# Performance work log

Measured on AMD Instinct MI355X. Metric: run time of the kernel, lower is better.

The kernel has to match this reference:

```python
import jax, jax.numpy as jnp
import numpy as np

B, T, U, L, C = 2048, 100, 512, 3, 10


def setup_inputs() -> dict:
    key = jax.random.key(0)
    ks = jax.random.split(key, 2 + 3 * L + 2)
    x = jax.random.normal(ks[0], (B, T, 1), dtype=jnp.float32)
    mask = jax.random.randint(ks[1], (B, T), 0, 2) > 0
    inp = {"x": x, "mask": mask}
    in_dim = 1
    s = 2
    for l in range(L):
        # Keras LSTM kernel layout: gates ordered [i, f, g(candidate), o]
        inp[f"W{l}"] = jax.random.normal(ks[s], (in_dim, 4 * U), dtype=jnp.float32) * 0.05
        inp[f"U{l}"] = jax.random.normal(ks[s + 1], (U, 4 * U), dtype=jnp.float32) * 0.05
        b = np.zeros((4 * U,), dtype=np.float32)
        b[U:2 * U] = 1.0  # unit_forget_bias (Keras default)
        inp[f"b{l}"] = jnp.asarray(b)
        in_dim = U
        s += 2
    inp["Wd"] = jax.random.normal(ks[s], (U, C), dtype=jnp.float32) * 0.05
    inp["bd"] = jnp.zeros((C,), dtype=jnp.float32)
    return inp


def _lstm_step(x_t, h, c, W, Uw, b):
    z = x_t @ W + h @ Uw + b  # [B, 4U]
    i, f, g, o = jnp.split(z, 4, axis=-1)
    i = jax.nn.sigmoid(i)
    f = jax.nn.sigmoid(f)
    g = jnp.tanh(g)
    o = jax.nn.sigmoid(o)
    c_new = f * c + i * g
    h_new = o * jnp.tanh(c_new)
    return h_new, c_new


def reference(x, mask, W0, U0, b0, W1, U1, b1, W2, U2, b2, Wd, bd):
    params = [(W0, U0, b0), (W1, U1, b1), (W2, U2, b2)]
    xt = jnp.swapaxes(x, 0, 1)        # [T, B, 1]
    mt = jnp.swapaxes(mask, 0, 1)     # [T, B]
    Bsz = x.shape[0]
    init = tuple((jnp.zeros((Bsz, U), x.dtype), jnp.zeros((Bsz, U), x.dtype)) for _ in range(L))

    def scan_fn(carry, inp_t):
        x_t, m_t = inp_t
        m = m_t[:, None]  # [B, 1]
        new_states = []
        layer_in = x_t
        for (h, c), (W, Uw, b) in zip(carry, params):
            h_new, c_new = _lstm_step(layer_in, h, c, W, Uw, b)
            # Keras mask semantics: masked steps carry state/output forward
            h_new = jnp.where(m, h_new, h)
            c_new = jnp.where(m, c_new, c)
            new_states.append((h_new, c_new))
            layer_in = h_new
        return tuple(new_states), None

    final, _ = jax.lax.scan(scan_fn, init, (xt, mt))
    h_top = final[-1][0]  # [B, U]
    logits = h_top @ Wd + bd
    return jax.nn.softmax(logits, axis=-1)
```

## Files before the change

kernel.cpp:

```cpp
#include <hip/hip_runtime.h>
#include <cstdint>
#include <cstddef>

#define B_   2048
#define T_   100
#define U_   512
#define NG_  2048
#define C_   10

typedef __attribute__((ext_vector_type(8))) short   short8;
typedef __attribute__((ext_vector_type(4))) float   floatx4;
typedef unsigned short ushort_t;

__device__ inline ushort_t f2bf(float f){
  unsigned u = __float_as_uint(f);
  unsigned r = (u + 0x7FFFu + ((u >> 16) & 1u)) >> 16;
  return (ushort_t)r;
}
__device__ inline float bf2f(ushort_t b){ return __uint_as_float(((unsigned)b) << 16); }

__device__ inline float sigm(float x){ return 1.0f / (1.0f + __expf(-x)); }
__device__ inline float tanh_fast(float x){
  float a = fabsf(x);
  float e = __expf(-2.0f * a);
  float r = (1.0f - e) / (1.0f + e);
  return copysignf(r, x);
}

__device__ inline int orig_col(int p){
  int Tt  = p >> 7;
  int loc = p & 127;
  int half = loc >> 6;
  int loc2 = loc & 63;
  int gate = loc2 >> 4;
  int uu   = (half << 4) | (loc2 & 15);
  return gate * U_ + Tt * 32 + uu;
}

#define AS1(p) ((const __attribute__((address_space(1))) void*)(p))
#define AS3(p) ((__attribute__((address_space(3))) void*)(p))

__global__ void convert_weights(
    const float* __restrict__ W0, const float* __restrict__ U0, const float* __restrict__ b0,
    const float* __restrict__ W1, const float* __restrict__ U1, const float* __restrict__ b1,
    const float* __restrict__ W2, const float* __restrict__ U2, const float* __restrict__ b2,
    ushort_t* __restrict__ Bt0, ushort_t* __restrict__ Bt1, ushort_t* __restrict__ Bt2,
    float* __restrict__ W0p, float* __restrict__ biasp)
{
  const int N0 = NG_ * 512;
  const int N1 = NG_ * 1024;
  const int total = N0 + 2 * N1 + NG_ + 3 * NG_;
  int idx = blockIdx.x * 256 + threadIdx.x;
  if (idx >= total) return;

  if (idx < N0){
    int p = idx >> 9, k = idx & 511;
    Bt0[idx] = f2bf(U0[(size_t)k * NG_ + orig_col(p)]);
  } else if (idx < N0 + N1){
    int j = idx - N0; int p = j >> 10, k = j & 1023;
    int oc = orig_col(p);
    float v = (k < 512) ? W1[(size_t)k * NG_ + oc] : U1[(size_t)(k - 512) * NG_ + oc];
    Bt1[j] = f2bf(v);
  } else if (idx < N0 + 2 * N1){
    int j = idx - N0 - N1; int p = j >> 10, k = j & 1023;
    int oc = orig_col(p);
    float v = (k < 512) ? W2[(size_t)k * NG_ + oc] : U2[(size_t)(k - 512) * NG_ + oc];
    Bt2[j] = f2bf(v);
  } else if (idx < N0 + 2 * N1 + NG_){
    int p = idx - N0 - 2 * N1;
    W0p[p] = W0[orig_col(p)];
  } else {
    int j = idx - N0 - 2 * N1 - NG_;
    int l = j >> 11, p = j & 2047;
    const float* bs = (l == 0) ? b0 : (l == 1) ? b1 : b2;
    biasp[j] = bs[orig_col(p)];
  }
}

template<int LAYER>
__device__ __forceinline__ void do_task(
    const ushort_t* __restrict__ A0,
    const ushort_t* __restrict__ A1,
    const ushort_t* __restrict__ Bt,
    const float* __restrict__ biasp,
    const float* __restrict__ W0p,
    const float* __restrict__ x,
    const int* __restrict__ mask,
    float* __restrict__ cbuf,
    const ushort_t* __restrict__ hprev,
    ushort_t* __restrict__ hout,
    int t, int mt, int nt,
    ushort_t* tA, ushort_t* tB)
{
  constexpr int NPHASE = (LAYER == 0) ? 1 : 2;
  constexpr bool IS_L0 = (LAYER == 0);
  constexpr int K = NPHASE * 512;

  const int tid  = threadIdx.x;
  const int wv   = tid >> 6;
  const int lane = tid & 63;
  const int qd   = lane >> 4;
  const int l16  = lane & 15;
  const int wave_m = wv >> 1;
  const int wave_n = wv & 1;
  const int m0 = mt * 128, n0 = nt * 128;

  int srow[4], scol[4];
  #pragma unroll
  for (int cc2 = 0; cc2 < 4; ++cc2){
    int i = cc2 * 256 + wv * 64 + lane;
    srow[cc2] = i >> 3;
    scol[cc2] = ((i & 7) + (i >> 3)) & 7;
  }

  int aoff[2][4], boff[2][4];
  #pragma unroll
  for (int ks = 0; ks < 2; ++ks){
    #pragma unroll
    for (int w = 0; w < 4; ++w){
      int Ra = wave_m * 64 + w * 16 + l16;
      int Rb = wave_n * 64 + w * 16 + l16;
      int q  = ks * 4 + qd;
      aoff[ks][w] = Ra * 64 + ((q - Ra) & 7) * 8;
      boff[ks][w] = Rb * 64 + ((q - Rb) & 7) * 8;
    }
  }

  floatx4 acc[4][4];
  #pragma unroll
  for (int i = 0; i < 4; ++i)
    #pragma unroll
    for (int j = 0; j < 4; ++j) acc[i][j] = (floatx4){0.f, 0.f, 0.f, 0.f};

  #pragma unroll
  for (int ph = 0; ph < NPHASE; ++ph){
    const ushort_t* A = (NPHASE == 2 && ph == 1) ? A1 : A0;
    for (int k0 = 0; k0 < 512; k0 += 64){
      #pragma unroll
      for (int cc2 = 0; cc2 < 4; ++cc2){
        int ibase = cc2 * 256 + wv * 64;
        const ushort_t* ga = A + (size_t)(m0 + srow[cc2]) * U_ + k0 + scol[cc2] * 8;
        __builtin_amdgcn_global_load_lds(AS1(ga), AS3(&tA[ibase * 8]), 16, 0, 0);
        const ushort_t* gb = Bt + (size_t)(n0 + srow[cc2]) * K + ph * 512 + k0 + scol[cc2] * 8;
        __builtin_amdgcn_global_load_lds(AS1(gb), AS3(&tB[ibase * 8]), 16, 0, 0);
      }
      __syncthreads();

      #pragma unroll
      for (int ks = 0; ks < 2; ++ks){
        short8 af[4], bfr[4];
        #pragma unroll
        for (int wm = 0; wm < 4; ++wm)
          af[wm] = *(const short8*)&tA[aoff[ks][wm]];
        #pragma unroll
        for (int wn = 0; wn < 4; ++wn)
          bfr[wn] = *(const short8*)&tB[boff[ks][wn]];
        #pragma unroll
        for (int wm = 0; wm < 4; ++wm)
          #pragma unroll
          for (int wn = 0; wn < 4; ++wn)
            acc[wm][wn] = __builtin_amdgcn_mfma_f32_16x16x32_bf16(af[wm], bfr[wn], acc[wm][wn], 0, 0, 0);
      }
      __syncthreads();
    }
  }

  const int u  = nt * 32 + wave_n * 16 + l16;
  const int pb = nt * 128 + wave_n * 64 + l16;
  const float bi = biasp[pb], bf_ = biasp[pb + 16], bg = biasp[pb + 32], bo = biasp[pb + 48];
  float wi = 0.f, wf = 0.f, wg = 0.f, wo = 0.f;
  if (IS_L0){ wi = W0p[pb]; wf = W0p[pb + 16]; wg = W0p[pb + 32]; wo = W0p[pb + 48]; }

  #pragma unroll
  for (int wm = 0; wm < 4; ++wm){
    #pragma unroll
    for (int reg = 0; reg < 4; ++reg){
      int b = m0 + wave_m * 64 + wm * 16 + qd * 4 + reg;
      float zi = acc[wm][0][reg] + bi;
      float zf = acc[wm][1][reg] + bf_;
      float zg = acc[wm][2][reg] + bg;
      float zo = acc[wm][3][reg] + bo;
      if (IS_L0){
        float xv = x[(size_t)b * T_ + t];
        zi += xv * wi; zf += xv * wf; zg += xv * wg; zo += xv * wo;
      }
      int mk = mask[(size_t)b * T_ + t];
      size_t su = (size_t)b * U_ + u;
      float c_old = cbuf[su];
      float i_ = sigm(zi), f_ = sigm(zf), g_ = tanh_fast(zg), o_ = sigm(zo);
      float c_new = f_ * c_old + i_ * g_;
      float h_new = o_ * tanh_fast(c_new);
      ushort_t hb = mk ? f2bf(h_new) : hprev[su];
      cbuf[su] = mk ? c_new : c_old;
      hout[su] = hb;
    }
  }
}

__global__ __launch_bounds__(256, 3) void lstm_phase(
    const ushort_t* __restrict__ Bt0, const ushort_t* __restrict__ Bt1,
    const ushort_t* __restrict__ Bt2, const float* __restrict__ biasp,
    const float* __restrict__ W0p, const float* __restrict__ x,
    const int* __restrict__ mask,
    ushort_t* h00, ushort_t* h01, ushort_t* h10, ushort_t* h11,
    ushort_t* h20, ushort_t* h21,
    float* c0, float* c1, float* c2,
    int s)
{
  __shared__ __align__(16) ushort_t tA[128 * 64];
  __shared__ __align__(16) ushort_t tB[128 * 64];

  const int lin  = blockIdx.x;
  const int task = lin >> 8;
  const int tile = lin & 255;
  const int mt = tile >> 4, nt = tile & 15;

  ushort_t* h0[2] = {h00, h01};
  ushort_t* h1[2] = {h10, h11};
  ushort_t* h2[2] = {h20, h21};

  if (task == 0){
    if (s >= 100) return;
    int t = s, p = t & 1;
    do_task<0>(h0[p], nullptr, Bt0, biasp, W0p, x, mask,
               c0, h0[p], h0[p ^ 1], t, mt, nt, tA, tB);
  } else if (task == 1){
    if (s < 1 || s > 100) return;
    int t = s - 1, p = t & 1;
    do_task<1>(h0[p ^ 1], h1[p], Bt1, biasp + NG_, nullptr, x, mask,
               c1, h1[p], h1[p ^ 1], t, mt, nt, tA, tB);
  } else {
    if (s < 2) return;
    int t = s - 2, p = t & 1;
    do_task<2>(h1[p ^ 1], h2[p], Bt2, biasp + 2 * NG_, nullptr, x, mask,
               c2, h2[p], h2[p ^ 1], t, mt, nt, tA, tB);
  }
}

__global__ __launch_bounds__(256) void head_softmax(
    const ushort_t* __restrict__ h2, const float* __restrict__ Wd,
    const float* __restrict__ bd, float* __restrict__ out)
{
  int wv = threadIdx.x >> 6, lane = threadIdx.x & 63;
  int row = blockIdx.x * 4 + wv;
  const ushort_t* hr = h2 + (size_t)row * U_;

  float acc[C_];
  #pragma unroll
  for (int c = 0; c < C_; ++c) acc[c] = 0.f;

  short8 hv = *(const short8*)&hr[lane * 8];
  #pragma unroll
  for (int j = 0; j < 8; ++j){
    float hf = bf2f((ushort_t)hv[j]);
    int k = lane * 8 + j;
    #pragma unroll
    for (int c = 0; c < C_; ++c) acc[c] += hf * Wd[k * C_ + c];
  }
  #pragma unroll
  for (int c = 0; c < C_; ++c){
    float v = acc[c];
    #pragma unroll
    for (int off = 32; off > 0; off >>= 1) v += __shfl_xor(v, off);
    acc[c] = v + bd[c];
  }
  float mx = acc[0];
  #pragma unroll
  for (int c = 1; c < C_; ++c) mx = fmaxf(mx, acc[c]);
  float e[C_]; float s = 0.f;
  #pragma unroll
  for (int c = 0; c < C_; ++c){ e[c] = __expf(acc[c] - mx); s += e[c]; }
  float inv = 1.0f / s;
  if (lane == 0){
    #pragma unroll
    for (int c = 0; c < C_; ++c) out[(size_t)row * C_ + c] = e[c] * inv;
  }
}

extern "C" void kernel_launch(void* const* d_in, const int* in_sizes, int n_in,
                              void* d_out, int out_size, void* d_ws, size_t ws_size,
                              hipStream_t stream)
{
  const float* x  = (const float*)d_in[0];
  const int*  mask= (const int*)  d_in[1];
  const float* W0 = (const float*)d_in[2];
  const float* U0 = (const float*)d_in[3];
  const float* b0 = (const float*)d_in[4];
  const float* W1 = (const float*)d_in[5];
  const float* U1 = (const float*)d_in[6];
  const float* b1 = (const float*)d_in[7];
  const float* W2 = (const float*)d_in[8];
  const float* U2 = (const float*)d_in[9];
  const float* b2 = (const float*)d_in[10];
  const float* Wd = (const float*)d_in[11];
  const float* bd = (const float*)d_in[12];
  float* out = (float*)d_out;

  char* ws = (char*)d_ws;
  size_t off = 0;
  auto alloc = [&](size_t sz) -> char* {
    char* p = ws + off; off = (off + sz + 255) & ~(size_t)255; return p;
  };
  ushort_t* Bt0  = (ushort_t*)alloc((size_t)NG_ * 512 * 2);
  ushort_t* Bt1  = (ushort_t*)alloc((size_t)NG_ * 1024 * 2);
  ushort_t* Bt2  = (ushort_t*)alloc((size_t)NG_ * 1024 * 2);
  float*    W0p  = (float*)alloc((size_t)NG_ * 4);
  float*    biasp= (float*)alloc((size_t)3 * NG_ * 4);

  const size_t hsz = (size_t)B_ * U_ * 2;
  const size_t csz = (size_t)B_ * U_ * 4;
  char* state = alloc(6 * hsz + 3 * csz);
  ushort_t* hb[3][2]; float* cb[3];
  {
    char* pp = state;
    for (int l = 0; l < 3; ++l)
      for (int par = 0; par < 2; ++par){ hb[l][par] = (ushort_t*)pp; pp += hsz; }
    for (int l = 0; l < 3; ++l){ cb[l] = (float*)pp; pp += csz; }
  }

  hipMemsetAsync(state, 0, 6 * hsz + 3 * csz, stream);

  const int total = NG_ * 512 + 2 * NG_ * 1024 + NG_ + 3 * NG_;
  convert_weights<<<(total + 255) / 256, 256, 0, stream>>>(
      W0, U0, b0, W1, U1, b1, W2, U2, b2, Bt0, Bt1, Bt2, W0p, biasp);

  for (int s = 0; s < 102; ++s){
    lstm_phase<<<768, 256, 0, stream>>>(
        Bt0, Bt1, Bt2, biasp, W0p, x, mask,
        hb[0][0], hb[0][1], hb[1][0], hb[1][1], hb[2][0], hb[2][1],
        cb[0], cb[1], cb[2], s);
  }

  head_softmax<<<B_ / 4, 256, 0, stream>>>(hb[2][0], Wd, bd, out);
}
```

Before: 3.480 ms.

## Use wider 128x256 tiles for layers 1-2 and reorder block scheduling

```diff
diff --git a/kernel.cpp b/kernel.cpp
--- a/kernel.cpp
+++ b/kernel.cpp
@@ -77,10 +77,8 @@
   }
 }
 
-template<int LAYER>
-__device__ __forceinline__ void do_task(
+__device__ __forceinline__ void do_task_l0(
     const ushort_t* __restrict__ A0,
-    const ushort_t* __restrict__ A1,
     const ushort_t* __restrict__ Bt,
     const float* __restrict__ biasp,
     const float* __restrict__ W0p,
@@ -92,10 +90,6 @@
     int t, int mt, int nt,
     ushort_t* tA, ushort_t* tB)
 {
-  constexpr int NPHASE = (LAYER == 0) ? 1 : 2;
-  constexpr bool IS_L0 = (LAYER == 0);
-  constexpr int K = NPHASE * 512;
-
   const int tid  = threadIdx.x;
   const int wv   = tid >> 6;
   const int lane = tid & 63;
@@ -107,10 +101,10 @@
 
   int srow[4], scol[4];
   #pragma unroll
-  for (int cc2 = 0; cc2 < 4; ++cc2){
-    int i = cc2 * 256 + wv * 64 + lane;
-    srow[cc2] = i >> 3;
-    scol[cc2] = ((i & 7) + (i >> 3)) & 7;
+  for (int g = 0; g < 4; ++g){
+    int i = g * 256 + tid;
+    srow[g] = i >> 3;
+    scol[g] = ((i & 7) + (i >> 3)) & 7;
   }
 
   int aoff[2][4], boff[2][4];
@@ -132,59 +126,49 @@
     #pragma unroll
     for (int j = 0; j < 4; ++j) acc[i][j] = (floatx4){0.f, 0.f, 0.f, 0.f};
 
-  #pragma unroll
-  for (int ph = 0; ph < NPHASE; ++ph){
-    const ushort_t* A = (NPHASE == 2 && ph == 1) ? A1 : A0;
-    for (int k0 = 0; k0 < 512; k0 += 64){
-      #pragma unroll
-      for (int cc2 = 0; cc2 < 4; ++cc2){
-        int ibase = cc2 * 256 + wv * 64;
-        const ushort_t* ga = A + (size_t)(m0 + srow[cc2]) * U_ + k0 + scol[cc2] * 8;
-        __builtin_amdgcn_global_load_lds(AS1(ga), AS3(&tA[ibase * 8]), 16, 0, 0);
-        const ushort_t* gb = Bt + (size_t)(n0 + srow[cc2]) * K + ph * 512 + k0 + scol[cc2] * 8;
-        __builtin_amdgcn_global_load_lds(AS1(gb), AS3(&tB[ibase * 8]), 16, 0, 0);
-      }
-      __syncthreads();
-
-      #pragma unroll
-      for (int ks = 0; ks < 2; ++ks){
-        short8 af[4], bfr[4];
-        #pragma unroll
-        for (int wm = 0; wm < 4; ++wm)
-          af[wm] = *(const short8*)&tA[aoff[ks][wm]];
+  for (int k0 = 0; k0 < 512; k0 += 64){
+    #pragma unroll
+    for (int g = 0; g < 4; ++g){
+      int ibase = g * 256 + wv * 64;
+      const ushort_t* ga = A0 + (size_t)(m0 + srow[g]) * U_ + k0 + scol[g] * 8;
+      __builtin_amdgcn_global_load_lds(AS1(ga), AS3(&tA[ibase * 8]), 16, 0, 0);
+      const ushort_t* gb = Bt + (size_t)(n0 + srow[g]) * 512 + k0 + scol[g] * 8;
+      __builtin_amdgcn_global_load_lds(AS1(gb), AS3(&tB[ibase * 8]), 16, 0, 0);
+    }
+    __syncthreads();
+
+    #pragma unroll
+    for (int ks = 0; ks < 2; ++ks){
+      short8 af[4], bfr[4];
+      #pragma unroll
+      for (int wm = 0; wm < 4; ++wm) af[wm] = *(const short8*)&tA[aoff[ks][wm]];
+      #pragma unroll
+      for (int wn = 0; wn < 4; ++wn) bfr[wn] = *(const short8*)&tB[boff[ks][wn]];
+      #pragma unroll
+      for (int wm = 0; wm < 4; ++wm)
         #pragma unroll
         for (int wn = 0; wn < 4; ++wn)
-          bfr[wn] = *(const short8*)&tB[boff[ks][wn]];
-        #pragma unroll
-        for (int wm = 0; wm < 4; ++wm)
-          #pragma unroll
-          for (int wn = 0; wn < 4; ++wn)
-            acc[wm][wn] = __builtin_amdgcn_mfma_f32_16x16x32_bf16(af[wm], bfr[wn], acc[wm][wn], 0, 0, 0);
-      }
-      __syncthreads();
-    }
+          acc[wm][wn] = __builtin_amdgcn_mfma_f32_16x16x32_bf16(af[wm], bfr[wn], acc[wm][wn], 0, 0, 0);
+    }
+    __syncthreads();
   }
 
   const int u  = nt * 32 + wave_n * 16 + l16;
   const int pb = nt * 128 + wave_n * 64 + l16;
   const float bi = biasp[pb], bf_ = biasp[pb + 16], bg = biasp[pb + 32], bo = biasp[pb + 48];
-  float wi = 0.f, wf = 0.f, wg = 0.f, wo = 0.f;
-  if (IS_L0){ wi = W0p[pb]; wf = W0p[pb + 16]; wg = W0p[pb + 32]; wo = W0p[pb + 48]; }
+  const float wi = W0p[pb], wf = W0p[pb + 16], wg = W0p[pb + 32], wo = W0p[pb + 48];
 
   #pragma unroll
   for (int wm = 0; wm < 4; ++wm){
     #pragma unroll
     for (int reg = 0; reg < 4; ++reg){
       int b = m0 + wave_m * 64 + wm * 16 + qd * 4 + reg;
-      float zi = acc[wm][0][reg] + bi;
-      float zf = acc[wm][1][reg] + bf_;
-      float zg = acc[wm][2][reg] + bg;
-      float zo = acc[wm][3][reg] + bo;
-      if (IS_L0){
-        float xv = x[(size_t)b * T_ + t];
-        zi += xv * wi; zf += xv * wf; zg += xv * wg; zo += xv * wo;
-      }
+      float xv = x[(size_t)b * T_ + t];
       int mk = mask[(size_t)b * T_ + t];
+      float zi = acc[wm][0][reg] + bi + xv * wi;
+      float zf = acc[wm][1][reg] + bf_ + xv * wf;
+      float zg = acc[wm][2][reg] + bg + xv * wg;
+      float zo = acc[wm][3][reg] + bo + xv * wo;
       size_t su = (size_t)b * U_ + u;
       float c_old = cbuf[su];
       float i_ = sigm(zi), f_ = sigm(zf), g_ = tanh_fast(zg), o_ = sigm(zo);
@@ -197,7 +181,132 @@
   }
 }
 
-__global__ __launch_bounds__(256, 3) void lstm_phase(
+__device__ __forceinline__ void do_task_wide(
+    const ushort_t* __restrict__ A0,
+    const ushort_t* __restrict__ A1,
+    const ushort_t* __restrict__ Bt,
+    const float* __restrict__ biasp,
+    const int* __restrict__ mask,
+    float* __restrict__ cbuf,
+    const ushort_t* __restrict__ hprev,
+    ushort_t* __restrict__ hout,
+    int t, int mt, int nt2,
+    ushort_t* tA, ushort_t* tB)
+{
+  const int tid  = threadIdx.x;
+  const int wv   = tid >> 6;
+  const int lane = tid & 63;
+  const int qd   = lane >> 4;
+  const int l16  = lane & 15;
+  const int wave_m = wv >> 1;
+  const int wave_n = wv & 1;
+  const int m0 = mt * 128, n0 = nt2 * 256;
+
+  int srA[4], scA[4], srB[8], scB[8];
+  #pragma unroll
+  for (int g = 0; g < 4; ++g){
+    int i = g * 256 + tid;
+    srA[g] = i >> 3; scA[g] = ((i & 7) + (i >> 3)) & 7;
+  }
+  #pragma unroll
+  for (int g = 0; g < 8; ++g){
+    int i = g * 256 + tid;
+    srB[g] = i >> 3; scB[g] = ((i & 7) + (i >> 3)) & 7;
+  }
+
+  int aoff[2][4], boff[2][8];
+  #pragma unroll
+  for (int ks = 0; ks < 2; ++ks){
+    int q = ks * 4 + qd;
+    #pragma unroll
+    for (int w = 0; w < 4; ++w){
+      int Ra = wave_m * 64 + w * 16 + l16;
+      aoff[ks][w] = Ra * 64 + ((q - Ra) & 7) * 8;
+    }
+    #pragma unroll
+    for (int w = 0; w < 8; ++w){
+      int Rb = wave_n * 128 + w * 16 + l16;
+      boff[ks][w] = Rb * 64 + ((q - Rb) & 7) * 8;
+    }
+  }
+
+  floatx4 acc[4][8];
+  #pragma unroll
+  for (int i = 0; i < 4; ++i)
+    #pragma unroll
+    for (int j = 0; j < 8; ++j) acc[i][j] = (floatx4){0.f, 0.f, 0.f, 0.f};
+
+  #pragma unroll 1
+  for (int ph = 0; ph < 2; ++ph){
+    const ushort_t* A = ph ? A1 : A0;
+    for (int k0 = 0; k0 < 512; k0 += 64){
+      #pragma unroll
+      for (int g = 0; g < 4; ++g){
+        int ibase = g * 256 + wv * 64;
+        const ushort_t* ga = A + (size_t)(m0 + srA[g]) * U_ + k0 + scA[g] * 8;
+        __builtin_amdgcn_global_load_lds(AS1(ga), AS3(&tA[ibase * 8]), 16, 0, 0);
+      }
+      #pragma unroll
+      for (int g = 0; g < 8; ++g){
+        int ibase = g * 256 + wv * 64;
+        const ushort_t* gb = Bt + (size_t)(n0 + srB[g]) * 1024 + ph * 512 + k0 + scB[g] * 8;
+        __builtin_amdgcn_global_load_lds(AS1(gb), AS3(&tB[ibase * 8]), 16, 0, 0);
+      }
+      __syncthreads();
+
+      #pragma unroll
+      for (int ks = 0; ks < 2; ++ks){
+        short8 af[4], bfr[8];
+        #pragma unroll
+        for (int wm = 0; wm < 4; ++wm) af[wm] = *(const short8*)&tA[aoff[ks][wm]];
+        #pragma unroll
+        for (int wn = 0; wn < 8; ++wn) bfr[wn] = *(const short8*)&tB[boff[ks][wn]];
+        #pragma unroll
+        for (int wm = 0; wm < 4; ++wm)
+          #pragma unroll
+          for (int wn = 0; wn < 8; ++wn)
+            acc[wm][wn] = __builtin_amdgcn_mfma_f32_16x16x32_bf16(af[wm], bfr[wn], acc[wm][wn], 0, 0, 0);
+      }
+      __syncthreads();
+    }
+  }
+
+  const int ntp = nt2 * 2 + wave_n;
+  float bb[2][4];
+  #pragma unroll
+  for (int h2 = 0; h2 < 2; ++h2){
+    int pb = ntp * 128 + h2 * 64 + l16;
+    #pragma unroll
+    for (int g = 0; g < 4; ++g) bb[h2][g] = biasp[pb + g * 16];
+  }
+
+  #pragma unroll
+  for (int wm = 0; wm < 4; ++wm){
+    #pragma unroll
+    for (int reg = 0; reg < 4; ++reg){
+      int b = m0 + wave_m * 64 + wm * 16 + qd * 4 + reg;
+      int mk = mask[(size_t)b * T_ + t];
+      #pragma unroll
+      for (int h2 = 0; h2 < 2; ++h2){
+        int u = ntp * 32 + h2 * 16 + l16;
+        float zi = acc[wm][h2 * 4 + 0][reg] + bb[h2][0];
+        float zf = acc[wm][h2 * 4 + 1][reg] + bb[h2][1];
+        float zg = acc[wm][h2 * 4 + 2][reg] + bb[h2][2];
+        float zo = acc[wm][h2 * 4 + 3][reg] + bb[h2][3];
+        size_t su = (size_t)b * U_ + u;
+        float c_old = cbuf[su];
+        float i_ = sigm(zi), f_ = sigm(zf), g_ = tanh_fast(zg), o_ = sigm(zo);
+        float c_new = f_ * c_old + i_ * g_;
+        float h_new = o_ * tanh_fast(c_new);
+        ushort_t hbv = mk ? f2bf(h_new) : hprev[su];
+        cbuf[su] = mk ? c_new : c_old;
+        hout[su] = hbv;
+      }
+    }
+  }
+}
+
+__global__ __launch_bounds__(256, 2) void lstm_phase(
     const ushort_t* __restrict__ Bt0, const ushort_t* __restrict__ Bt1,
     const ushort_t* __restrict__ Bt2, const float* __restrict__ biasp,
     const float* __restrict__ W0p, const float* __restrict__ x,
@@ -208,32 +317,29 @@
     int s)
 {
   __shared__ __align__(16) ushort_t tA[128 * 64];
-  __shared__ __align__(16) ushort_t tB[128 * 64];
-
-  const int lin  = blockIdx.x;
-  const int task = lin >> 8;
-  const int tile = lin & 255;
-  const int mt = tile >> 4, nt = tile & 15;
+  __shared__ __align__(16) ushort_t tB[256 * 64];
+
+  const int lin = blockIdx.x;
 
   ushort_t* h0[2] = {h00, h01};
   ushort_t* h1[2] = {h10, h11};
   ushort_t* h2[2] = {h20, h21};
 
-  if (task == 0){
-    if (s >= 100) return;
-    int t = s, p = t & 1;
-    do_task<0>(h0[p], nullptr, Bt0, biasp, W0p, x, mask,
-               c0, h0[p], h0[p ^ 1], t, mt, nt, tA, tB);
-  } else if (task == 1){
+  if (lin < 128){
     if (s < 1 || s > 100) return;
     int t = s - 1, p = t & 1;
-    do_task<1>(h0[p ^ 1], h1[p], Bt1, biasp + NG_, nullptr, x, mask,
-               c1, h1[p], h1[p ^ 1], t, mt, nt, tA, tB);
+    do_task_wide(h0[p ^ 1], h1[p], Bt1, biasp + NG_, mask,
+                 c1, h1[p], h1[p ^ 1], t, lin >> 3, lin & 7, tA, tB);
+  } else if (lin < 256){
+    if (s < 2) return;
+    int j = lin - 128, t = s - 2, p = t & 1;
+    do_task_wide(h1[p ^ 1], h2[p], Bt2, biasp + 2 * NG_, mask,
+                 c2, h2[p], h2[p ^ 1], t, j >> 3, j & 7, tA, tB);
   } else {
-    if (s < 2) return;
-    int t = s - 2, p = t & 1;
-    do_task<2>(h1[p ^ 1], h2[p], Bt2, biasp + 2 * NG_, nullptr, x, mask,
-               c2, h2[p], h2[p ^ 1], t, mt, nt, tA, tB);
+    if (s >= 100) return;
+    int tile = lin - 256, t = s, p = t & 1;
+    do_task_l0(h0[p], Bt0, biasp, W0p, x, mask,
+               c0, h0[p], h0[p ^ 1], t, tile >> 4, tile & 15, tA, tB);
   }
 }
 
@@ -325,7 +431,7 @@
       W0, U0, b0, W1, U1, b1, W2, U2, b2, Bt0, Bt1, Bt2, W0p, biasp);
 
   for (int s = 0; s < 102; ++s){
-    lstm_phase<<<768, 256, 0, stream>>>(
+    lstm_phase<<<512, 256, 0, stream>>>(
         Bt0, Bt1, Bt2, biasp, W0p, x, mask,
         hb[0][0], hb[0][1], hb[1][0], hb[1][1], hb[2][0], hb[2][1],
         cb[0], cb[1], cb[2], s);
```

New measurement: 4.695 ms. 1.35x slower.

## Double-buffer LDS tiles with K=32 steps to overlap global loads with MFMA

Applied to the files above, without the earlier changes.

```diff
diff --git a/kernel.cpp b/kernel.cpp
--- a/kernel.cpp
+++ b/kernel.cpp
@@ -95,6 +95,7 @@
   constexpr int NPHASE = (LAYER == 0) ? 1 : 2;
   constexpr bool IS_L0 = (LAYER == 0);
   constexpr int K = NPHASE * 512;
+  constexpr int NIT = NPHASE * 16;
 
   const int tid  = threadIdx.x;
   const int wv   = tid >> 6;
@@ -105,64 +106,73 @@
   const int wave_n = wv & 1;
   const int m0 = mt * 128, n0 = nt * 128;
 
-  int srow[4], scol[4];
-  #pragma unroll
-  for (int cc2 = 0; cc2 < 4; ++cc2){
-    int i = cc2 * 256 + wv * 64 + lane;
-    srow[cc2] = i >> 3;
-    scol[cc2] = ((i & 7) + (i >> 3)) & 7;
-  }
-
-  int aoff[2][4], boff[2][4];
-  #pragma unroll
-  for (int ks = 0; ks < 2; ++ks){
-    #pragma unroll
-    for (int w = 0; w < 4; ++w){
-      int Ra = wave_m * 64 + w * 16 + l16;
-      int Rb = wave_n * 64 + w * 16 + l16;
-      int q  = ks * 4 + qd;
-      aoff[ks][w] = Ra * 64 + ((q - Ra) & 7) * 8;
-      boff[ks][w] = Rb * 64 + ((q - Rb) & 7) * 8;
+  int abase[2], bbase[2];
+  #pragma unroll
+  for (int g = 0; g < 2; ++g){
+    int i = g * 256 + tid;
+    int r = i >> 2;
+    int sc = ((i & 3) + (r >> 1)) & 3;
+    abase[g] = (m0 + r) * U_ + sc * 8;
+    bbase[g] = (n0 + r) * K + sc * 8;
+  }
+
+  int aoff[4], boff[4];
+  #pragma unroll
+  for (int w = 0; w < 4; ++w){
+    int Ra = wave_m * 64 + w * 16 + l16;
+    int Rb = wave_n * 64 + w * 16 + l16;
+    aoff[w] = Ra * 32 + ((qd - (Ra >> 1)) & 3) * 8;
+    boff[w] = Rb * 32 + ((qd - (Rb >> 1)) & 3) * 8;
+  }
+
+  floatx4 acc[4][4];
+  #pragma unroll
+  for (int i = 0; i < 4; ++i)
+    #pragma unroll
+    for (int j = 0; j < 4; ++j) acc[i][j] = (floatx4){0.f, 0.f, 0.f, 0.f};
+
+  {
+    const ushort_t* A = A0;
+    #pragma unroll
+    for (int g = 0; g < 2; ++g){
+      int ibase = g * 256 + wv * 64;
+      __builtin_amdgcn_global_load_lds(AS1(A + abase[g]), AS3(&tA[ibase * 8]), 16, 0, 0);
+      __builtin_amdgcn_global_load_lds(AS1(Bt + bbase[g]), AS3(&tB[ibase * 8]), 16, 0, 0);
     }
   }
 
-  floatx4 acc[4][4];
-  #pragma unroll
-  for (int i = 0; i < 4; ++i)
-    #pragma unroll
-    for (int j = 0; j < 4; ++j) acc[i][j] = (floatx4){0.f, 0.f, 0.f, 0.f};
-
-  #pragma unroll
-  for (int ph = 0; ph < NPHASE; ++ph){
-    const ushort_t* A = (NPHASE == 2 && ph == 1) ? A1 : A0;
-    for (int k0 = 0; k0 < 512; k0 += 64){
+  #pragma unroll 2
+  for (int it = 0; it < NIT; ++it){
+    __syncthreads();
+
+    if (it + 1 < NIT){
+      int nit = it + 1;
+      int nk  = (nit & 15) * 32;
+      const ushort_t* A = (NPHASE == 2 && nit >= 16) ? A1 : A0;
+      int ak = nk;
+      int bk = (NPHASE == 2 && nit >= 16) ? 512 + nk : nk;
+      ushort_t* dA = tA + (nit & 1) * (128 * 32);
+      ushort_t* dB = tB + (nit & 1) * (128 * 32);
       #pragma unroll
-      for (int cc2 = 0; cc2 < 4; ++cc2){
-        int ibase = cc2 * 256 + wv * 64;
-        const ushort_t* ga = A + (size_t)(m0 + srow[cc2]) * U_ + k0 + scol[cc2] * 8;
-        __builtin_amdgcn_global_load_lds(AS1(ga), AS3(&tA[ibase * 8]), 16, 0, 0);
-        const ushort_t* gb = Bt + (size_t)(n0 + srow[cc2]) * K + ph * 512 + k0 + scol[cc2] * 8;
-        __builtin_amdgcn_global_load_lds(AS1(gb), AS3(&tB[ibase * 8]), 16, 0, 0);
+      for (int g = 0; g < 2; ++g){
+        int ibase = g * 256 + wv * 64;
+        __builtin_amdgcn_global_load_lds(AS1(A + abase[g] + ak), AS3(&dA[ibase * 8]), 16, 0, 0);
+        __builtin_amdgcn_global_load_lds(AS1(Bt + bbase[g] + bk), AS3(&dB[ibase * 8]), 16, 0, 0);
       }
-      __syncthreads();
-
+    }
+
+    const ushort_t* sA = tA + (it & 1) * (128 * 32);
+    const ushort_t* sB = tB + (it & 1) * (128 * 32);
+    short8 af[4], bfr[4];
+    #pragma unroll
+    for (int wm = 0; wm < 4; ++wm) af[wm] = *(const short8*)&sA[aoff[wm]];
+    #pragma unroll
+    for (int wn = 0; wn < 4; ++wn) bfr[wn] = *(const short8*)&sB[boff[wn]];
+    #pragma unroll
+    for (int wm = 0; wm < 4; ++wm)
       #pragma unroll
-      for (int ks = 0; ks < 2; ++ks){
-        short8 af[4], bfr[4];
-        #pragma unroll
-        for (int wm = 0; wm < 4; ++wm)
-          af[wm] = *(const short8*)&tA[aoff[ks][wm]];
-        #pragma unroll
-        for (int wn = 0; wn < 4; ++wn)
-          bfr[wn] = *(const short8*)&tB[boff[ks][wn]];
-        #pragma unroll
-        for (int wm = 0; wm < 4; ++wm)
-          #pragma unroll
-          for (int wn = 0; wn < 4; ++wn)
-            acc[wm][wn] = __builtin_amdgcn_mfma_f32_16x16x32_bf16(af[wm], bfr[wn], acc[wm][wn], 0, 0, 0);
-      }
-      __syncthreads();
-    }
+      for (int wn = 0; wn < 4; ++wn)
+        acc[wm][wn] = __builtin_amdgcn_mfma_f32_16x16x32_bf16(af[wm], bfr[wn], acc[wm][wn], 0, 0, 0);
   }
 
   const int u  = nt * 32 + wave_n * 16 + l16;
@@ -207,8 +217,8 @@
     float* c0, float* c1, float* c2,
     int s)
 {
-  __shared__ __align__(16) ushort_t tA[128 * 64];
-  __shared__ __align__(16) ushort_t tB[128 * 64];
+  __shared__ __align__(16) ushort_t tA[2 * 128 * 32];
+  __shared__ __align__(16) ushort_t tB[2 * 128 * 32];
 
   const int lin  = blockIdx.x;
   const int task = lin >> 8;
```

Result: slower. 4.409 ms (+26.7%).
